# Optimization experiments

Hardware: AMD Instinct MI355X
Metric: run time of the kernel (lower is better)

The kernel has to match this reference:

```python
import jax, jax.numpy as jnp
import numpy as np

B, C, H, W = 4, 64, 64, 64
INTER, HALF = C // 8, C // 2  # 8, 32


def setup_inputs() -> dict:
    key = jax.random.key(0)
    ks = jax.random.split(key, 10)
    return {
        "x": jax.random.normal(ks[0], (B, C, H, W), jnp.float32),
        "Wf": jax.random.normal(ks[1], (INTER, C), jnp.float32) * 0.1,
        "bf": jax.random.normal(ks[2], (INTER,), jnp.float32) * 0.1,
        "Wg": jax.random.normal(ks[3], (INTER, C), jnp.float32) * 0.1,
        "bg": jax.random.normal(ks[4], (INTER,), jnp.float32) * 0.1,
        "Wh": jax.random.normal(ks[5], (HALF, C), jnp.float32) * 0.1,
        "bh": jax.random.normal(ks[6], (HALF,), jnp.float32) * 0.1,
        "Wv": jax.random.normal(ks[7], (C, HALF), jnp.float32) * 0.1,
        "bv": jax.random.normal(ks[8], (C,), jnp.float32) * 0.1,
        "gamma": jax.random.normal(ks[9], (1,), jnp.float32),
    }


def reference(x, Wf, bf, Wg, bg, Wh, bh, Wv, bv, gamma):
    b, c, h, w = x.shape
    n = h * w
    xf = x.reshape(b, c, n)  # [B, C, N]
    # 1x1 convs are channel matmuls
    f = jnp.einsum('oc,bcn->bno', Wf, xf) + bf            # [B, N, inter] (key, transposed)
    g = jnp.einsum('oc,bcn->bon', Wg, xf) + bg[:, None]   # [B, inter, N] (query)
    hv = jnp.einsum('oc,bcn->bon', Wh, xf) + bh[:, None]  # [B, half, N]  (value)
    # attn[b,i,j] = softmax_j( f[b,i,:] . g[b,:,j] )  (no scaling, as in source)
    attn = jax.nn.softmax(jnp.einsum('bno,bom->bnm', f, g), axis=-1)  # [B, N, N]
    # o[b,c,i] = sum_j hv[b,c,j] * attn[b,i,j]
    o = jnp.einsum('bcm,bnm->bcn', hv, attn)              # [B, half, N]
    o = jnp.einsum('oc,bcn->bon', Wv, o) + bv[:, None]    # [B, C, N]
    return gamma * o.reshape(b, c, h, w) + x
```

## Files before the change

kernel.cpp:

```cpp
#include <hip/hip_runtime.h>
#include <math.h>

#define BB 4
#define CC 64
#define NN 4096
#define IND 8
#define HF 32
#define QBLK 32
#define THREADS 512
#define WAVES 8
#define MBLK 32
#define MCHUNK (NN/WAVES)
#define NBLK (MCHUNK/MBLK)

typedef __attribute__((ext_vector_type(8))) short bf16x8;
typedef __attribute__((ext_vector_type(4))) float f32x4;

static __device__ __forceinline__ unsigned short f2bf(float x) {
    unsigned int u = __float_as_uint(x);
    u = (u + 0x7FFFu + ((u >> 16) & 1u)) >> 16;
    return (unsigned short)u;
}
static __device__ __forceinline__ float bf2f(unsigned short h) {
    return __uint_as_float(((unsigned int)h) << 16);
}
static __device__ __forceinline__ unsigned int pk2(float lo, float hi) {
    return (unsigned int)f2bf(lo) | ((unsigned int)f2bf(hi) << 16);
}
static __device__ __forceinline__ float ex2(float x) {
    return __builtin_amdgcn_exp2f(x);
}


__global__ __launch_bounds__(128) void proj_kernel(
    const float* __restrict__ x,
    const float* __restrict__ Wf, const float* __restrict__ bf,
    const float* __restrict__ Wg, const float* __restrict__ bg,
    const float* __restrict__ Wh, const float* __restrict__ bh,
    unsigned short* __restrict__ fpk,
    unsigned short* __restrict__ gpk,
    unsigned short* __restrict__ vblk)
{
    __shared__ float swT[CC][8];

    int tid = threadIdx.x;
    int bx  = blockIdx.x;
    int og  = bx >> 7;
    int p   = (bx & 127) * 128 + tid;
    int b = p >> 12;
    int n = p & (NN - 1);
    const float* xp = x + (size_t)b * CC * NN + n;

    const float* W;
    const float* bias;
    if (og == 0)      { W = Wf; bias = bf; }
    else if (og == 1) { W = Wg; bias = bg; }
    else              { W = Wh + (og - 2) * 8 * CC; bias = bh + (og - 2) * 8; }

    {
        float4 wv = *(const float4*)(W + tid * 4);
        int o = (tid * 4) >> 6;
        int c0 = (tid * 4) & 63;
        swT[c0 + 0][o] = wv.x;
        swT[c0 + 1][o] = wv.y;
        swT[c0 + 2][o] = wv.z;
        swT[c0 + 3][o] = wv.w;
    }

    float xv[CC];
    #pragma unroll
    for (int c = 0; c < CC; c++) xv[c] = xp[(size_t)c * NN];
    #pragma unroll
    for (int c = 0; c < CC; c++) asm volatile("" : "+v"(xv[c]));

    __syncthreads();

    float a[8];
    #pragma unroll
    for (int o = 0; o < 8; o++) a[o] = bias[o];
    #pragma unroll
    for (int c = 0; c < CC; c++) {
        float4 w0 = *(const float4*)&swT[c][0];
        float4 w1 = *(const float4*)&swT[c][4];
        float v = xv[c];
        a[0] += w0.x * v; a[1] += w0.y * v; a[2] += w0.z * v; a[3] += w0.w * v;
        a[4] += w1.x * v; a[5] += w1.y * v; a[6] += w1.z * v; a[7] += w1.w * v;
    }

    const float LOG2E = 1.4426950408889634f;
    size_t base = (size_t)b * NN + n;

    if (og == 0) {
        union { unsigned short s[16]; uint4 q[2]; } fo;
        #pragma unroll
        for (int o = 0; o < 8; o++) {
            unsigned short hi = f2bf(a[o]);
            unsigned short lo = f2bf(a[o] - bf2f(hi));
            fo.s[o] = hi; fo.s[8 + o] = lo;
        }
        uint4* fdst = (uint4*)(fpk + base * 16);
        fdst[0] = fo.q[0]; fdst[1] = fo.q[1];
    } else if (og == 1) {
        union { unsigned short s[32]; uint4 q[4]; } go;
        #pragma unroll
        for (int o = 0; o < 8; o++) {
            float gsc = a[o] * LOG2E;
            unsigned short hi = f2bf(gsc);
            unsigned short lo = f2bf(gsc - bf2f(hi));
            go.s[o] = hi; go.s[8 + o] = hi; go.s[16 + o] = lo; go.s[24 + o] = lo;
        }
        uint4* gdst = (uint4*)(gpk + base * 32);
        #pragma unroll
        for (int k = 0; k < 4; k++) gdst[k] = go.q[k];
    } else {
        int m5 = n & 31;
        int code = (m5 & 3) | (((m5 >> 4) & 1) << 2) | (((m5 >> 2) & 3) << 3);
        int mb = (n >> 5);
        int h0 = (og - 2) * 8;
        int hg = h0 >> 4;
        unsigned short* vp = vblk + (size_t)b * (NN/32) * 1024
                           + (size_t)mb * 1024 + hg * 512 + code;
        #pragma unroll
        for (int o = 0; o < 8; o++)
            vp[((h0 + o) & 15) * 32] = f2bf(a[o]);
    }
}

__global__ __launch_bounds__(THREADS, 4) void attn_kernel(
    const unsigned short* __restrict__ fpk,
    const unsigned short* __restrict__ gpk,
    const unsigned short* __restrict__ vblk,
    const float* __restrict__ Wv, const float* __restrict__ bv,
    const float* __restrict__ gamma,
    const float* __restrict__ x, float* __restrict__ out)
{
    __shared__ float sl[WAVES][QBLK][HF + 1];

    int tid  = threadIdx.x;
    int wave = tid >> 6;
    int lane = tid & 63;
    int c15  = lane & 15;
    int g4   = lane >> 4;

    int l  = (blockIdx.x & 7) * 64 + (blockIdx.x >> 3);
    int b  = l >> 7;
    int n0 = (l & 127) * QBLK;

    bf16x8 bq[2];
    #pragma unroll
    for (int qg = 0; qg < 2; qg++)
        bq[qg] = *(const bf16x8*)(fpk
                  + ((size_t)(b * NN + n0 + qg*16 + c15)) * 16 + (g4 & 1) * 8);

    f32x4 zero4 = {0.f, 0.f, 0.f, 0.f};
    f32x4 acc[2][2];
    float Lacc[2] = {0.f, 0.f};
    #pragma unroll
    for (int qg = 0; qg < 2; qg++) { acc[qg][0] = zero4; acc[qg][1] = zero4; }

    const unsigned short* gsrc = gpk  + (size_t)b * NN * 32;
    const unsigned short* vsrc = vblk + (size_t)b * (NN/32) * 1024;
    int mbase = wave * MCHUNK;
    int mb0   = wave * NBLK;

    bf16x8 akc[2], vbc[2];
    {
        int m0 = mbase;
        akc[0] = *(const bf16x8*)(gsrc + (size_t)(m0 + c15)      * 32 + g4*8);
        akc[1] = *(const bf16x8*)(gsrc + (size_t)(m0 + 16 + c15) * 32 + g4*8);
        const unsigned short* vb = vsrc + (size_t)mb0 * 1024 + c15*32 + g4*8;
        vbc[0] = *(const bf16x8*)(vb);
        vbc[1] = *(const bf16x8*)(vb + 512);
    }

    #pragma unroll 2
    for (int t = 0; t < NBLK; t++) {
        bf16x8 akn[2], vbn[2];
        if (t + 1 < NBLK) {
            int m1 = mbase + (t + 1) * MBLK;
            akn[0] = *(const bf16x8*)(gsrc + (size_t)(m1 + c15)      * 32 + g4*8);
            akn[1] = *(const bf16x8*)(gsrc + (size_t)(m1 + 16 + c15) * 32 + g4*8);
            const unsigned short* vb = vsrc + (size_t)(mb0 + t + 1) * 1024
                                     + c15*32 + g4*8;
            vbn[0] = *(const bf16x8*)(vb);
            vbn[1] = *(const bf16x8*)(vb + 512);
        }

        f32x4 sf[2][2];
        #pragma unroll
        for (int mg = 0; mg < 2; mg++)
            #pragma unroll
            for (int qg = 0; qg < 2; qg++)
                sf[qg][mg] = __builtin_amdgcn_mfma_f32_16x16x32_bf16(
                    akc[mg], bq[qg], zero4, 0, 0, 0);

        bf16x8 pa[2];
        #pragma unroll
        for (int qg = 0; qg < 2; qg++) {
            float e00 = ex2(sf[qg][0][0]), e01 = ex2(sf[qg][0][1]);
            float e02 = ex2(sf[qg][0][2]), e03 = ex2(sf[qg][0][3]);
            float e10 = ex2(sf[qg][1][0]), e11 = ex2(sf[qg][1][1]);
            float e12 = ex2(sf[qg][1][2]), e13 = ex2(sf[qg][1][3]);
            Lacc[qg] += ((e00 + e01) + (e02 + e03)) + ((e10 + e11) + (e12 + e13));
            union { unsigned int u[4]; bf16x8 v; } pp;
            pp.u[0] = pk2(e00, e01); pp.u[1] = pk2(e02, e03);
            pp.u[2] = pk2(e10, e11); pp.u[3] = pk2(e12, e13);
            pa[qg] = pp.v;
        }

        #pragma unroll
        for (int qg = 0; qg < 2; qg++)
            #pragma unroll
            for (int hg = 0; hg < 2; hg++)
                acc[qg][hg] = __builtin_amdgcn_mfma_f32_16x16x32_bf16(
                    pa[qg], vbc[hg], acc[qg][hg], 0, 0, 0);

        if (t + 1 < NBLK) {
            akc[0] = akn[0]; akc[1] = akn[1];
            vbc[0] = vbn[0]; vbc[1] = vbn[1];
        }
    }

    #pragma unroll
    for (int qg = 0; qg < 2; qg++)
        #pragma unroll
        for (int hg = 0; hg < 2; hg++)
            #pragma unroll
            for (int r = 0; r < 4; r++)
                sl[wave][qg*16 + g4*4 + r][hg*16 + c15] = acc[qg][hg][r];
    #pragma unroll
    for (int qg = 0; qg < 2; qg++) {
        float t = Lacc[qg];
        t += __shfl_xor(t, 16);
        t += __shfl_xor(t, 32);
        if (g4 == 0) sl[wave][qg*16 + c15][HF] = t;
    }
    __syncthreads();

    {
        int q = tid & 31;
        for (int col = tid >> 5; col < HF + 1; col += 16) {
            float s = sl[0][q][col];
            #pragma unroll
            for (int w2 = 1; w2 < WAVES; w2++) s += sl[w2][q][col];
            sl[0][q][col] = s;
        }
    }
    __syncthreads();

    int q  = tid & 31;
    int cb = tid >> 5;
    float rL = 1.f / sl[0][q][HF];
    float o_[HF];
    #pragma unroll
    for (int h = 0; h < HF; h++) o_[h] = sl[0][q][h] * rL;
    float gm = gamma[0];
    size_t obase = (size_t)b * CC * NN + n0 + q;
    for (int c = cb*4; c < cb*4 + 4; c++) {
        float v = bv[c];
        #pragma unroll
        for (int h = 0; h < HF; h++) v += Wv[c*HF + h] * o_[h];
        size_t a = obase + (size_t)c * NN;
        out[a] = gm * v + x[a];
    }
}

extern "C" void kernel_launch(void* const* d_in, const int* in_sizes, int n_in,
                              void* d_out, int out_size, void* d_ws, size_t ws_size,
                              hipStream_t stream) {
    const float* x     = (const float*)d_in[0];
    const float* Wf    = (const float*)d_in[1];
    const float* bf    = (const float*)d_in[2];
    const float* Wg    = (const float*)d_in[3];
    const float* bg    = (const float*)d_in[4];
    const float* Wh    = (const float*)d_in[5];
    const float* bh    = (const float*)d_in[6];
    const float* Wv    = (const float*)d_in[7];
    const float* bv    = (const float*)d_in[8];
    const float* gamma = (const float*)d_in[9];
    float* out = (float*)d_out;

    unsigned short* ws   = (unsigned short*)d_ws;
    unsigned short* fpk  = ws;
    unsigned short* gpk  = ws + (size_t)BB*NN*16;
    unsigned short* vblk = ws + (size_t)BB*NN*48;

    proj_kernel<<<(BB*NN/128)*6, 128, 0, stream>>>(x, Wf, bf, Wg, bg, Wh, bh,
                                                   fpk, gpk, vblk);
    attn_kernel<<<BB*(NN/QBLK), THREADS, 0, stream>>>(fpk, gpk, vblk,
                                                      Wv, bv, gamma, x, out);
}
```

Measured before the change: 32.93 us.

## Fuse projection outputs per block sharing an LDS-staged x tile

Projection now loads a 64-channel by 64-pixel tile of x into shared memory once per block and computes f, g and both value groups from it in separate waves, instead of launching six block groups that each re-read x. Value outputs are assembled in shared memory and written with coalesced 16-byte stores. This removes redundant global reads of x and scattered 2-byte stores, at the cost of fewer blocks, more LDS, and non-unrolled inner loops.

```diff
diff --git a/kernel.cpp b/kernel.cpp
--- a/kernel.cpp
+++ b/kernel.cpp
@@ -32,7 +32,7 @@
 }
 
 
-__global__ __launch_bounds__(128) void proj_kernel(
+__global__ __launch_bounds__(256) void proj_kernel(
     const float* __restrict__ x,
     const float* __restrict__ Wf, const float* __restrict__ bf,
     const float* __restrict__ Wg, const float* __restrict__ bg,
@@ -41,56 +41,50 @@
     unsigned short* __restrict__ gpk,
     unsigned short* __restrict__ vblk)
 {
-    __shared__ float swT[CC][8];
+    __shared__ float xtile[CC][65];
+    __shared__ float wT[CC][52];
+    __shared__ unsigned short vtile[2][1024];
 
     int tid = threadIdx.x;
     int bx  = blockIdx.x;
-    int og  = bx >> 7;
-    int p   = (bx & 127) * 128 + tid;
-    int b = p >> 12;
-    int n = p & (NN - 1);
-    const float* xp = x + (size_t)b * CC * NN + n;
-
-    const float* W;
-    const float* bias;
-    if (og == 0)      { W = Wf; bias = bf; }
-    else if (og == 1) { W = Wg; bias = bg; }
-    else              { W = Wh + (og - 2) * 8 * CC; bias = bh + (og - 2) * 8; }
-
+    int b   = bx >> 6;
+    int n0  = (bx & 63) * 64;
+
+    for (int idx = tid; idx < IND*CC; idx += 256) {
+        int o = idx >> 6, c = idx & 63;
+        wT[c][o]     = Wf[idx];
+        wT[c][8 + o] = Wg[idx];
+    }
+    for (int idx = tid; idx < HF*CC; idx += 256) {
+        int o = idx >> 6, c = idx & 63;
+        wT[c][16 + o] = Wh[idx];
+    }
     {
-        float4 wv = *(const float4*)(W + tid * 4);
-        int o = (tid * 4) >> 6;
-        int c0 = (tid * 4) & 63;
-        swT[c0 + 0][o] = wv.x;
-        swT[c0 + 1][o] = wv.y;
-        swT[c0 + 2][o] = wv.z;
-        swT[c0 + 3][o] = wv.w;
-    }
-
-    float xv[CC];
-    #pragma unroll
-    for (int c = 0; c < CC; c++) xv[c] = xp[(size_t)c * NN];
-    #pragma unroll
-    for (int c = 0; c < CC; c++) asm volatile("" : "+v"(xv[c]));
-
+        const float* xb = x + (size_t)b * CC * NN + n0;
+        for (int idx = tid; idx < CC*64; idx += 256) {
+            int c = idx >> 6, nl = idx & 63;
+            xtile[c][nl] = xb[(size_t)c * NN + nl];
+        }
+    }
     __syncthreads();
 
-    float a[8];
-    #pragma unroll
-    for (int o = 0; o < 8; o++) a[o] = bias[o];
-    #pragma unroll
-    for (int c = 0; c < CC; c++) {
-        float4 w0 = *(const float4*)&swT[c][0];
-        float4 w1 = *(const float4*)&swT[c][4];
-        float v = xv[c];
-        a[0] += w0.x * v; a[1] += w0.y * v; a[2] += w0.z * v; a[3] += w0.w * v;
-        a[4] += w1.x * v; a[5] += w1.y * v; a[6] += w1.z * v; a[7] += w1.w * v;
-    }
-
+    int wave = tid >> 6;
+    int nl   = tid & 63;
+    int n    = n0 + nl;
+    size_t base = (size_t)b * NN + n;
     const float LOG2E = 1.4426950408889634f;
-    size_t base = (size_t)b * NN + n;
-
-    if (og == 0) {
+
+    if (wave == 0) {
+        float a[8];
+        #pragma unroll
+        for (int o = 0; o < 8; o++) a[o] = bf[o];
+        for (int c = 0; c < CC; c++) {
+            float v = xtile[c][nl];
+            float4 w0 = *(const float4*)&wT[c][0];
+            float4 w1 = *(const float4*)&wT[c][4];
+            a[0] += w0.x*v; a[1] += w0.y*v; a[2] += w0.z*v; a[3] += w0.w*v;
+            a[4] += w1.x*v; a[5] += w1.y*v; a[6] += w1.z*v; a[7] += w1.w*v;
+        }
         union { unsigned short s[16]; uint4 q[2]; } fo;
         #pragma unroll
         for (int o = 0; o < 8; o++) {
@@ -100,7 +94,17 @@
         }
         uint4* fdst = (uint4*)(fpk + base * 16);
         fdst[0] = fo.q[0]; fdst[1] = fo.q[1];
-    } else if (og == 1) {
+    } else if (wave == 1) {
+        float a[8];
+        #pragma unroll
+        for (int o = 0; o < 8; o++) a[o] = bg[o];
+        for (int c = 0; c < CC; c++) {
+            float v = xtile[c][nl];
+            float4 w0 = *(const float4*)&wT[c][8];
+            float4 w1 = *(const float4*)&wT[c][12];
+            a[0] += w0.x*v; a[1] += w0.y*v; a[2] += w0.z*v; a[3] += w0.w*v;
+            a[4] += w1.x*v; a[5] += w1.y*v; a[6] += w1.z*v; a[7] += w1.w*v;
+        }
         union { unsigned short s[32]; uint4 q[4]; } go;
         #pragma unroll
         for (int o = 0; o < 8; o++) {
@@ -113,16 +117,35 @@
         #pragma unroll
         for (int k = 0; k < 4; k++) gdst[k] = go.q[k];
     } else {
-        int m5 = n & 31;
+        int hg = wave - 2;
+        int h0 = hg * 16;
+        float a[16];
+        #pragma unroll
+        for (int i = 0; i < 16; i++) a[i] = bh[h0 + i];
+        for (int c = 0; c < CC; c++) {
+            float v = xtile[c][nl];
+            #pragma unroll
+            for (int j = 0; j < 4; j++) {
+                float4 w = *(const float4*)&wT[c][16 + h0 + j*4];
+                a[j*4+0] += w.x*v; a[j*4+1] += w.y*v;
+                a[j*4+2] += w.z*v; a[j*4+3] += w.w*v;
+            }
+        }
+        int m5 = nl & 31;
         int code = (m5 & 3) | (((m5 >> 4) & 1) << 2) | (((m5 >> 2) & 3) << 3);
-        int mb = (n >> 5);
-        int h0 = (og - 2) * 8;
-        int hg = h0 >> 4;
-        unsigned short* vp = vblk + (size_t)b * (NN/32) * 1024
-                           + (size_t)mb * 1024 + hg * 512 + code;
-        #pragma unroll
-        for (int o = 0; o < 8; o++)
-            vp[((h0 + o) & 15) * 32] = f2bf(a[o]);
+        int mb = nl >> 5;
+        unsigned short* vp = &vtile[mb][hg * 512 + code];
+        #pragma unroll
+        for (int i = 0; i < 16; i++)
+            vp[i * 32] = f2bf(a[i]);
+    }
+    __syncthreads();
+
+    {
+        int lmb = tid >> 7;
+        int off = (tid & 127) * 8;
+        uint4 v = *(uint4*)&vtile[lmb][off];
+        *(uint4*)(vblk + ((size_t)(bx * 2 + lmb)) * 1024 + off) = v;
     }
 }
 
@@ -285,8 +308,8 @@
     unsigned short* gpk  = ws + (size_t)BB*NN*16;
     unsigned short* vblk = ws + (size_t)BB*NN*48;
 
-    proj_kernel<<<(BB*NN/128)*6, 128, 0, stream>>>(x, Wf, bf, Wg, bg, Wh, bh,
-                                                   fpk, gpk, vblk);
+    proj_kernel<<<BB*(NN/64), 256, 0, stream>>>(x, Wf, bf, Wg, bg, Wh, bh,
+                                                fpk, gpk, vblk);
     attn_kernel<<<BB*(NN/QBLK), THREADS, 0, stream>>>(fpk, gpk, vblk,
                                                       Wv, bv, gamma, x, out);
 }
```

Result: slower. 34.12 us (+3.6%).
